# Performance work log

Measured on AMD Instinct MI355X. Metric: run time of the kernel, lower is better.

The kernel has to match this reference:

```python
import jax, jax.numpy as jnp
import numpy as np
from jax import lax

LATENT = 128
CODEBOOK = 1024

def _conv(x, w, b):
    # NCHW conv, kernel OIHW, stride 1, padding 1 (same)
    y = lax.conv_general_dilated(x, w, (1, 1), ((1, 1), (1, 1)),
                                 dimension_numbers=('NCHW', 'OIHW', 'NCHW'))
    return y + b[None, :, None, None]

def _conv_transpose(x, w, b):
    # ConvTranspose2d(k=3, s=1, p=1) == conv with flipped kernel, in/out swapped, pad 1
    w_eff = jnp.flip(w, (2, 3)).transpose(1, 0, 2, 3)  # [Cin,Cout,3,3] -> [Cout,Cin,3,3]
    return _conv(x, w_eff, b)

def _maxpool2(x):
    return lax.reduce_window(x, -jnp.inf, lax.max, (1, 1, 2, 2), (1, 1, 2, 2), 'VALID')

def _upsample2(x):
    # F.interpolate(scale_factor=2), default nearest
    return jnp.repeat(jnp.repeat(x, 2, axis=2), 2, axis=3)

def setup_inputs() -> dict:
    key = jax.random.key(0)
    ks = jax.random.split(key, 20)
    f = jnp.float32
    inp = {
        'x': jax.random.uniform(ks[0], (8192, 1, 24, 24), dtype=f),
        'conv1_w': jax.random.normal(ks[1], (32, 1, 3, 3), f) * 0.1,
        'conv1_b': jnp.zeros((32,), f),
        'conv2_w': jax.random.normal(ks[2], (64, 32, 3, 3), f) * 0.05,
        'conv2_b': jnp.zeros((64,), f),
        'conv3_w': jax.random.normal(ks[3], (128, 64, 3, 3), f) * 0.04,
        'conv3_b': jnp.zeros((128,), f),
        'enc_fc_w': jax.random.normal(ks[4], (LATENT, 3 * 3 * 128), f) * 0.03,
        'enc_fc_b': jnp.zeros((LATENT,), f),
        'codebook': jax.random.normal(ks[5], (CODEBOOK, LATENT), f),
        'dec_fc_w': jax.random.normal(ks[6], (3 * 3 * 128, LATENT), f) * 0.09,
        'dec_fc_b': jnp.zeros((3 * 3 * 128,), f),
        'dct1_w': jax.random.normal(ks[7], (128, 64, 3, 3), f) * 0.03,  # [Cin,Cout,kh,kw]
        'dct1_b': jnp.zeros((64,), f),
        'dct2_w': jax.random.normal(ks[8], (64, 32, 3, 3), f) * 0.04,
        'dct2_b': jnp.zeros((32,), f),
        'dct3_w': jax.random.normal(ks[9], (32, 1, 3, 3), f) * 0.06,
        'dct3_b': jnp.zeros((1,), f),
    }
    return inp

def reference(x, conv1_w, conv1_b, conv2_w, conv2_b, conv3_w, conv3_b,
              enc_fc_w, enc_fc_b, codebook, dec_fc_w, dec_fc_b,
              dct1_w, dct1_b, dct2_w, dct2_b, dct3_w, dct3_b):
    # ---- Encoder ----
    h = _maxpool2(jax.nn.relu(_conv(x, conv1_w, conv1_b)))     # [B,32,12,12]
    h = _maxpool2(jax.nn.relu(_conv(h, conv2_w, conv2_b)))     # [B,64,6,6]
    h = _maxpool2(jax.nn.relu(_conv(h, conv3_w, conv3_b)))     # [B,128,3,3]
    z = h.reshape(-1, 3 * 3 * 128) @ enc_fc_w.T + enc_fc_b     # [B,128]
    # ---- Quantize (L2 nearest-codeword; matmul-trick distances, same argmin) ----
    d2 = (jnp.sum(z * z, axis=1, keepdims=True)
          - 2.0 * z @ codebook.T
          + jnp.sum(codebook * codebook, axis=1)[None, :])     # [B,K]
    idx = jnp.argmin(d2, axis=1)                               # [B]
    z_q = codebook[idx]                                        # [B,128]
    # ---- Decoder ----
    d = z_q @ dec_fc_w.T + dec_fc_b                            # [B,1152]
    d = d.reshape(-1, 128, 3, 3)
    d = _upsample2(jax.nn.relu(_conv_transpose(d, dct1_w, dct1_b)))  # [B,64,6,6]
    d = _upsample2(jax.nn.relu(_conv_transpose(d, dct2_w, dct2_b)))  # [B,32,12,12]
    d = _upsample2(jax.nn.relu(_conv_transpose(d, dct3_w, dct3_b)))  # [B,1,24,24]
    return d
```

## Files before the change

kernel.cpp:

```cpp
#include <hip/hip_runtime.h>

typedef __attribute__((ext_vector_type(8))) short short8;
typedef __attribute__((ext_vector_type(4))) float f32x4;
typedef unsigned short ushort_t;
typedef unsigned int uint_t;

#define OFF_W1R   0
#define OFF_BD2F  288
#define OFF_BD1F  18720
#define OFF_EWT   (18720+73728)
#define OFF_CT    (92448+147456)
#define OFF_CC    (239904+131072)
#define OFF_DWT   (370976+1024)
#define OFF_D1R   (372000+147456)
#define OFF_D2R   (519456+73728)
#define OFF_D3R   (593184+18432)
#define WS_WEIGHTS (611616+288)
#define OFF_W2BF  WS_WEIGHTS
#define OFF_W3BF  (OFF_W2BF+18432)
#define OFF_H     (OFF_W3BF+73728)
#define OFF_TABLE OFF_H
#define OFF_IDSN  (OFF_H+8192*1152)

__device__ __forceinline__ ushort_t f2bf(float v) {
  uint_t u = __float_as_uint(v);
  return (ushort_t)((u + 0x7FFFu + ((u >> 16) & 1u)) >> 16);
}
__device__ __forceinline__ float bf2f(ushort_t b) {
  return __uint_as_float(((uint_t)b) << 16);
}

__global__ void vq_prep(const float* __restrict__ conv1_w, const float* __restrict__ codebook,
                        const float* __restrict__ dec_fc_w, const float* __restrict__ dct3_w,
                        float* __restrict__ ws) {
  int i = blockIdx.x * blockDim.x + threadIdx.x;
  if (i >= WS_WEIGHTS) return;
  if (i < OFF_BD2F) {
    int tap = i >> 5, co = i & 31;
    ws[i] = conv1_w[co*9 + tap];
  } else if (i < OFF_CC) {
    return;
  } else if (i < OFF_DWT) {
    int k = i - OFF_CC;
    float s = 0.f;
    for (int j = 0; j < 128; ++j) { float v = codebook[k*128+j]; s += v*v; }
    ws[i] = s;
  } else if (i < OFF_D1R) {
    int l = i - OFF_DWT;
    int j = l % 1152, k = l / 1152;
    ws[i] = dec_fc_w[j*128 + k];
  } else if (i < OFF_D3R) {
    return;
  } else if (i < WS_WEIGHTS) {
    int l = i - OFF_D3R;
    int tap = l % 9, ci = l / 9;
    ws[i] = dct3_w[ci*9 + (8 - tap)];
  }
}

#define P2_N (92160 + 294912 + 262144 + 73728 + 18432)
__global__ void vq_prep2(const float* __restrict__ conv2_w, const float* __restrict__ conv3_w,
                         const float* __restrict__ enc_fc_w, const float* __restrict__ codebook,
                         const float* __restrict__ dct1_w, const float* __restrict__ dct2_w,
                         float* __restrict__ ws) {
  int i = blockIdx.x * blockDim.x + threadIdx.x;
  if (i >= P2_N) return;
  ushort_t* W2  = (ushort_t*)(ws + OFF_W2BF);
  ushort_t* W3  = (ushort_t*)(ws + OFF_W3BF);
  ushort_t* EW  = (ushort_t*)(ws + OFF_EWT);
  ushort_t* CB  = (ushort_t*)(ws + OFF_CT);
  ushort_t* BD1 = (ushort_t*)(ws + OFF_BD1F);
  ushort_t* BD2 = (ushort_t*)(ws + OFF_BD2F);
  if (i < 18432) {
    int tap = i >> 11, r = i & 2047, co = r >> 5, ch = r & 31;
    float v = conv2_w[(co*32 + ch)*9 + tap];
    ushort_t hb = f2bf(v);
    W2[i] = hb; W2[18432 + i] = f2bf(v - bf2f(hb));
  } else if (i < 92160) {
    int j = i - 18432;
    int tap = j >> 13, r = j & 8191, co = r >> 6, ch = r & 63;
    float v = conv3_w[(co*64 + ch)*9 + tap];
    ushort_t hb = f2bf(v);
    W3[j] = hb; W3[73728 + j] = f2bf(v - bf2f(hb));
  } else if (i < 387072) {
    int r = i - 92160;
    int p = r / 147456; r %= 147456;
    int kk = r & 31, n = (r >> 5) & 127, ks = r >> 12;
    float v = enc_fc_w[n*1152 + ks*32 + kk];
    ushort_t hb = f2bf(v);
    if (p == 0) EW[r] = hb; else EW[147456 + r] = f2bf(v - bf2f(hb));
  } else if (i < 649216) {
    int r = i - 387072;
    int p = r / 131072; r %= 131072;
    int kk = r & 31, cw = (r >> 5) & 1023, ks = r >> 15;
    float v = codebook[cw*128 + ks*32 + kk];
    ushort_t hb = f2bf(v);
    if (p == 0) CB[r] = hb; else CB[131072 + r] = f2bf(v - bf2f(hb));
  } else if (i < 722944) {
    int r = i - 649216;
    int co = r / 1152, k = r - co*1152;
    int tap = k >> 7, ci = k & 127;
    float v = dct1_w[(ci*64 + co)*9 + (8 - tap)];
    ushort_t hb = f2bf(v);
    BD1[r] = hb; BD1[73728 + r] = f2bf(v - bf2f(hb));
  } else {
    int r = i - 722944;
    int co = r / 576, k = r - co*576;
    int tap = k >> 6, ci = k & 63;
    float v = dct2_w[(ci*32 + co)*9 + (8 - tap)];
    ushort_t hb = f2bf(v);
    BD2[r] = hb; BD2[18432 + r] = f2bf(v - bf2f(hb));
  }
}

__global__ __launch_bounds__(256, 3) void vq_enc(
    const float* __restrict__ x,
    const float* __restrict__ b1, const float* __restrict__ b2, const float* __restrict__ b3,
    const float* __restrict__ ws, ushort_t* __restrict__ hhi, ushort_t* __restrict__ hlo)
{
  __shared__ ushort_t R0h[6272], R0l[6272];
  __shared__ ushort_t A2h[5120], A2l[5120];
  __shared__ float XT[624];
  const int t = threadIdx.x;
  const int b = blockIdx.x;

  for (int i = t; i < 3136; i += 256) { ((uint_t*)R0h)[i] = 0u; ((uint_t*)R0l)[i] = 0u; }
  for (int i = t; i < 2560; i += 256) { ((uint_t*)A2h)[i] = 0u; ((uint_t*)A2l)[i] = 0u; }
  const float* xb = x + (size_t)b * 576;
  for (int i = t; i < 624; i += 256) {
    int row = i / 26, c = i - row * 26;
    XT[i] = (c >= 1 && c <= 24) ? xb[row*24 + c - 1] : 0.f;
  }
  __syncthreads();

  {
    int cp = t & 15, g = t >> 4;
    int gy = g >> 2, gx = g & 3;
    float wgt[2][9], bs[2];
    #pragma unroll
    for (int c = 0; c < 2; ++c) {
      bs[c] = b1[2*cp + c];
      #pragma unroll
      for (int k = 0; k < 9; ++k) wgt[c][k] = ws[OFF_W1R + k*32 + 2*cp + c];
    }
    int quadc = cp >> 2, coff = (cp & 3) * 2;
    #pragma unroll
    for (int pr = 0; pr < 3; ++pr) {
      int Y = (gy*3 + pr)*2;
      float a0[2][6], a1[2][6];
      #pragma unroll
      for (int c = 0; c < 2; ++c)
        #pragma unroll
        for (int i = 0; i < 6; ++i) { a0[c][i] = 0.f; a1[c][i] = 0.f; }
      #pragma unroll
      for (int wy = 0; wy < 4; ++wy) {
        int ry = Y - 1 + wy;
        if (ry < 0 || ry > 23) continue;
        const float2* rp = (const float2*)&XT[ry*26 + gx*6];
        float r[8];
        #pragma unroll
        for (int k = 0; k < 4; ++k) { float2 p = rp[k]; r[2*k] = p.x; r[2*k+1] = p.y; }
        if (wy < 3) {
          #pragma unroll
          for (int c = 0; c < 2; ++c)
            #pragma unroll
            for (int xx = 0; xx < 6; ++xx)
              #pragma unroll
              for (int dx = 0; dx < 3; ++dx) a0[c][xx] += r[xx+dx] * wgt[c][wy*3+dx];
        }
        if (wy >= 1) {
          #pragma unroll
          for (int c = 0; c < 2; ++c)
            #pragma unroll
            for (int xx = 0; xx < 6; ++xx)
              #pragma unroll
              for (int dx = 0; dx < 3; ++dx) a1[c][xx] += r[xx+dx] * wgt[c][(wy-1)*3+dx];
        }
      }
      #pragma unroll
      for (int pc = 0; pc < 3; ++pc) {
        uint_t hi = 0, lo = 0;
        #pragma unroll
        for (int c = 0; c < 2; ++c) {
          float m = fmaxf(fmaxf(a0[c][2*pc], a0[c][2*pc+1]), fmaxf(a1[c][2*pc], a1[c][2*pc+1]));
          float v = m + bs[c]; v = v > 0.f ? v : 0.f;
          ushort_t hb = f2bf(v);
          ushort_t lb = f2bf(v - bf2f(hb));
          hi |= ((uint_t)hb) << (16*c);
          lo |= ((uint_t)lb) << (16*c);
        }
        int p = (gy*3 + pr + 1)*14 + (gx*3 + pc + 1);
        int base = quadc*1568 + p*8 + coff;
        ((uint_t*)R0h)[base >> 1] = hi;
        ((uint_t*)R0l)[base >> 1] = lo;
      }
    }
  }
  __syncthreads();

  const int lane = t & 63, quad = lane >> 4, col = lane & 15;
  const int wv = t >> 6;

  {
    const int h = wv & 1, p = wv >> 1;
    const ushort_t* W2 = (const ushort_t*)(ws + OFF_W2BF);
    int pA[5];
    #pragma unroll
    for (int mi = 0; mi < 5; ++mi) {
      int m = (h*5 + mi)*16 + col; if (m > 143) m = 143;
      int cell = m >> 2, sub = m & 3;
      int opy = cell / 6, opx = cell - opy*6;
      int y = 2*opy + (sub >> 1), xx = 2*opx + (sub & 1);
      pA[mi] = y*14 + xx;
    }
    f32x4 acc[5][2];
    #pragma unroll
    for (int mi = 0; mi < 5; ++mi) { acc[mi][0] = (f32x4)0.f; acc[mi][1] = (f32x4)0.f; }
    const int co0 = p*32 + col, co1 = co0 + 16;
    #pragma unroll
    for (int t9 = 0; t9 < 9; ++t9) {
      const int toff = (t9/3)*14 + (t9%3);
      int bidx = t9*2048 + quad*8;
      short8 Bh0 = *(const short8*)(W2 + bidx + co0*32);
      short8 Bh1 = *(const short8*)(W2 + bidx + co1*32);
      short8 Bl0 = *(const short8*)(W2 + 18432 + bidx + co0*32);
      short8 Bl1 = *(const short8*)(W2 + 18432 + bidx + co1*32);
      #pragma unroll
      for (int mi = 0; mi < 5; ++mi) {
        int a = quad*1568 + (pA[mi] + toff)*8;
        short8 Ah = *(const short8*)(R0h + a);
        short8 Al = *(const short8*)(R0l + a);
        acc[mi][0] = __builtin_amdgcn_mfma_f32_16x16x32_bf16(Al, Bh0, acc[mi][0], 0, 0, 0);
        acc[mi][0] = __builtin_amdgcn_mfma_f32_16x16x32_bf16(Ah, Bl0, acc[mi][0], 0, 0, 0);
        acc[mi][0] = __builtin_amdgcn_mfma_f32_16x16x32_bf16(Ah, Bh0, acc[mi][0], 0, 0, 0);
        acc[mi][1] = __builtin_amdgcn_mfma_f32_16x16x32_bf16(Al, Bh1, acc[mi][1], 0, 0, 0);
        acc[mi][1] = __builtin_amdgcn_mfma_f32_16x16x32_bf16(Ah, Bl1, acc[mi][1], 0, 0, 0);
        acc[mi][1] = __builtin_amdgcn_mfma_f32_16x16x32_bf16(Ah, Bh1, acc[mi][1], 0, 0, 0);
      }
    }
    #pragma unroll
    for (int mi = 0; mi < 5; ++mi) {
      int cell = (h*5 + mi)*4 + quad;
      if (cell < 36) {
        int opy = cell / 6, opx = cell - opy*6;
        int p2 = (opy+1)*10 + (opx+1);
        #pragma unroll
        for (int j = 0; j < 2; ++j) {
          int ch = j ? co1 : co0;
          f32x4 a = acc[mi][j];
          float v = fmaxf(fmaxf(a.x, a.y), fmaxf(a.z, a.w)) + b2[ch];
          v = v > 0.f ? v : 0.f;
          ushort_t hb = f2bf(v);
          int wa = (ch >> 3)*640 + p2*8 + (ch & 7);
          A2h[wa] = hb;
          A2l[wa] = f2bf(v - bf2f(hb));
        }
      }
    }
  }
  __syncthreads();

  {
    const ushort_t* W3 = (const ushort_t*)(ws + OFF_W3BF);
    int pA[3];
    #pragma unroll
    for (int mt = 0; mt < 3; ++mt) {
      int m = mt*16 + col; if (m > 35) m = 35;
      int cell = m >> 2, sub = m & 3;
      int opy = cell / 3, opx = cell - opy*3;
      int y = 2*opy + (sub >> 1), xx = 2*opx + (sub & 1);
      pA[mt] = y*10 + xx;
    }
    f32x4 acc[3][2];
    #pragma unroll
    for (int mt = 0; mt < 3; ++mt) { acc[mt][0] = (f32x4)0.f; acc[mt][1] = (f32x4)0.f; }
    const int co0 = wv*16 + col, co1 = co0 + 64;
    #pragma unroll
    for (int ks = 0; ks < 18; ++ks) {
      const int t9 = ks >> 1, half = ks & 1, ch0 = half*32;
      const int toff = (t9/3)*10 + (t9%3);
      const int grp = half*4 + quad;
      int bidx = t9*8192 + ch0 + quad*8;
      short8 Bh0 = *(const short8*)(W3 + bidx + co0*64);
      short8 Bh1 = *(const short8*)(W3 + bidx + co1*64);
      short8 Bl0 = *(const short8*)(W3 + 73728 + bidx + co0*64);
      short8 Bl1 = *(const short8*)(W3 + 73728 + bidx + co1*64);
      #pragma unroll
      for (int mt = 0; mt < 3; ++mt) {
        int a = grp*640 + (pA[mt] + toff)*8;
        short8 Ah = *(const short8*)(A2h + a);
        short8 Al = *(const short8*)(A2l + a);
        acc[mt][0] = __builtin_amdgcn_mfma_f32_16x16x32_bf16(Al, Bh0, acc[mt][0], 0, 0, 0);
        acc[mt][0] = __builtin_amdgcn_mfma_f32_16x16x32_bf16(Ah, Bl0, acc[mt][0], 0, 0, 0);
        acc[mt][0] = __builtin_amdgcn_mfma_f32_16x16x32_bf16(Ah, Bh0, acc[mt][0], 0, 0, 0);
        acc[mt][1] = __builtin_amdgcn_mfma_f32_16x16x32_bf16(Al, Bh1, acc[mt][1], 0, 0, 0);
        acc[mt][1] = __builtin_amdgcn_mfma_f32_16x16x32_bf16(Ah, Bl1, acc[mt][1], 0, 0, 0);
        acc[mt][1] = __builtin_amdgcn_mfma_f32_16x16x32_bf16(Ah, Bh1, acc[mt][1], 0, 0, 0);
      }
    }
    ushort_t* hb_ = hhi + (size_t)b * 1152;
    ushort_t* lb_ = hlo + (size_t)b * 1152;
    #pragma unroll
    for (int mt = 0; mt < 3; ++mt) {
      int cell = mt*4 + quad;
      if (cell < 9) {
        #pragma unroll
        for (int j = 0; j < 2; ++j) {
          int ch = j ? co1 : co0;
          f32x4 a = acc[mt][j];
          float v = fmaxf(fmaxf(a.x, a.y), fmaxf(a.z, a.w)) + b3[ch];
          v = v > 0.f ? v : 0.f;
          ushort_t hb2 = f2bf(v);
          hb_[ch*9 + cell] = hb2;
          lb_[ch*9 + cell] = f2bf(v - bf2f(hb2));
        }
      }
    }
  }
}

__global__ __launch_bounds__(256, 4) void vq_fc_argmin(
    const float* __restrict__ efb, const float* __restrict__ ws,
    const ushort_t* __restrict__ hhi, const ushort_t* __restrict__ hlo,
    int* __restrict__ ids)
{
  __shared__ float ZL[16*132];
  __shared__ float WVs[64];
  __shared__ int   WIs[64];
  const int t = threadIdx.x;
  const int sb = blockIdx.x * 16;
  const int lane = t & 63, wv = t >> 6;
  const int col = lane & 15, quad = lane >> 4;

  const ushort_t* EW  = (const ushort_t*)(ws + OFF_EWT);
  const ushort_t* CBB = (const ushort_t*)(ws + OFF_CT);

  f32x4 acc0 = (f32x4)0.f, acc1 = (f32x4)0.f;
  const size_t hrow = (size_t)(sb + col) * 1152 + quad*8;
  #pragma unroll 4
  for (int ks = 0; ks < 36; ++ks) {
    short8 Ah = *(const short8*)(hhi + hrow + ks*32);
    short8 Al = *(const short8*)(hlo + hrow + ks*32);
    int n0 = wv*32 + col, n1 = n0 + 16;
    const ushort_t* bp0 = EW + (ks*128 + n0)*32 + quad*8;
    const ushort_t* bp1 = EW + (ks*128 + n1)*32 + quad*8;
    short8 Bh0 = *(const short8*)(bp0);
    short8 Bl0 = *(const short8*)(bp0 + 147456);
    short8 Bh1 = *(const short8*)(bp1);
    short8 Bl1 = *(const short8*)(bp1 + 147456);
    acc0 = __builtin_amdgcn_mfma_f32_16x16x32_bf16(Al, Bh0, acc0, 0, 0, 0);
    acc0 = __builtin_amdgcn_mfma_f32_16x16x32_bf16(Ah, Bl0, acc0, 0, 0, 0);
    acc0 = __builtin_amdgcn_mfma_f32_16x16x32_bf16(Ah, Bh0, acc0, 0, 0, 0);
    acc1 = __builtin_amdgcn_mfma_f32_16x16x32_bf16(Al, Bh1, acc1, 0, 0, 0);
    acc1 = __builtin_amdgcn_mfma_f32_16x16x32_bf16(Ah, Bl1, acc1, 0, 0, 0);
    acc1 = __builtin_amdgcn_mfma_f32_16x16x32_bf16(Ah, Bh1, acc1, 0, 0, 0);
  }
  {
    int n0 = wv*32 + col, n1 = n0 + 16;
    float bs0 = efb[n0], bs1 = efb[n1];
    #pragma unroll
    for (int r = 0; r < 4; ++r) {
      int m = quad*4 + r;
      ZL[m*132 + n0] = acc0[r] + bs0;
      ZL[m*132 + n1] = acc1[r] + bs1;
    }
  }
  __syncthreads();

  short8 zAh[4], zAl[4];
  #pragma unroll
  for (int ks = 0; ks < 4; ++ks) {
    const float* zp = &ZL[col*132 + ks*32 + quad*8];
    float4 z0 = *(const float4*)zp;
    float4 z1 = *(const float4*)(zp + 4);
    float zv[8] = {z0.x, z0.y, z0.z, z0.w, z1.x, z1.y, z1.z, z1.w};
    ushort_t ph[8], pl[8];
    #pragma unroll
    for (int e = 0; e < 8; ++e) {
      ushort_t hb = f2bf(zv[e]);
      ph[e] = hb; pl[e] = f2bf(zv[e] - bf2f(hb));
    }
    zAh[ks] = *(const short8*)ph;
    zAl[ks] = *(const short8*)pl;
  }

  float bestv[4]; int besti[4];
  #pragma unroll
  for (int r = 0; r < 4; ++r) { bestv[r] = 3.4e38f; besti[r] = 0; }
  for (int c4 = 0; c4 < 4; ++c4) {
    f32x4 dacc[4];
    #pragma unroll
    for (int nn = 0; nn < 4; ++nn) dacc[nn] = (f32x4)0.f;
    #pragma unroll
    for (int ks = 0; ks < 4; ++ks) {
      #pragma unroll
      for (int nn = 0; nn < 4; ++nn) {
        int cw = (wv*16 + c4*4 + nn)*16 + col;
        const ushort_t* bp = CBB + (size_t)(ks*1024 + cw)*32 + quad*8;
        short8 Bh = *(const short8*)bp;
        short8 Bl = *(const short8*)(bp + 131072);
        dacc[nn] = __builtin_amdgcn_mfma_f32_16x16x32_bf16(zAl[ks], Bh, dacc[nn], 0, 0, 0);
        dacc[nn] = __builtin_amdgcn_mfma_f32_16x16x32_bf16(zAh[ks], Bl, dacc[nn], 0, 0, 0);
        dacc[nn] = __builtin_amdgcn_mfma_f32_16x16x32_bf16(zAh[ks], Bh, dacc[nn], 0, 0, 0);
      }
    }
    #pragma unroll
    for (int nn = 0; nn < 4; ++nn) {
      int cw = (wv*16 + c4*4 + nn)*16 + col;
      float ccv = ws[OFF_CC + cw];
      #pragma unroll
      for (int r = 0; r < 4; ++r) {
        float dist = ccv - 2.f*dacc[nn][r];
        if (dist < bestv[r]) { bestv[r] = dist; besti[r] = cw; }
      }
    }
  }

  #pragma unroll
  for (int r = 0; r < 4; ++r) {
    float v = bestv[r]; int ii = besti[r];
    #pragma unroll
    for (int off = 8; off >= 1; off >>= 1) {
      float v2 = __shfl_xor(v, off); int i2 = __shfl_xor(ii, off);
      if (v2 < v || (v2 == v && i2 < ii)) { v = v2; ii = i2; }
    }
    if (col == 0) {
      int m = quad*4 + r;
      WVs[wv*16 + m] = v; WIs[wv*16 + m] = ii;
    }
  }
  __syncthreads();
  if (t < 16) {
    float v = WVs[t]; int ii = WIs[t];
    #pragma unroll
    for (int w2 = 1; w2 < 4; ++w2) {
      float v2 = WVs[w2*16 + t]; int i2 = WIs[w2*16 + t];
      if (v2 < v || (v2 == v && i2 < ii)) { v = v2; ii = i2; }
    }
    ids[sb + t] = ii;
  }
}

__global__ __launch_bounds__(256, 4) void vq_dec_table(
    const float* __restrict__ codebook, const float* __restrict__ decb,
    const float* __restrict__ d1b, const float* __restrict__ d2b, const float* __restrict__ d3b,
    const float* __restrict__ ws, float* __restrict__ table)
{
  __shared__ float POOL[8008];
  __shared__ float PS[1536];
  __shared__ float ZQ[128];
  ushort_t* FAh = (ushort_t*)POOL;
  ushort_t* FAl = FAh + 3400;
  ushort_t* GAh = (ushort_t*)(POOL + 3400);
  ushort_t* GAl = GAh + 4608;
  float* R2 = POOL;

  const int t = threadIdx.x;
  const int cw = blockIdx.x;
  const int lane = t & 63, wv = t >> 6;
  const int col = lane & 15, quad = lane >> 4;

  for (int i = t; i < 8008; i += 256) POOL[i] = 0.f;
  if (t < 128) ZQ[t] = codebook[(size_t)cw*128 + t];
  __syncthreads();

  #pragma unroll
  for (int p = 0; p < 5; ++p) {
    int j = t + p*256;
    if (j < 1152) {
      float a0 = decb[j];
      const float* wb = ws + OFF_DWT + j;
      #pragma unroll 4
      for (int k = 0; k < 128; ++k) a0 += wb[k*1152] * ZQ[k];
      int ci = j / 9, rem = j - ci*9;
      int pix = ((rem/3)+1)*5 + (rem%3) + 1;
      ushort_t hb = f2bf(a0);
      FAh[pix*136 + ci] = hb;
      FAl[pix*136 + ci] = f2bf(a0 - bf2f(hb));
    }
  }
  __syncthreads();

  const ushort_t* BD1 = (const ushort_t*)(ws + OFF_BD1F);
  f32x4 acc1 = (f32x4)0.f;
  {
    const int m9 = col < 9 ? col : 8;
    const int oy = m9/3, ox = m9 - oy*3;
    const int co = wv*16 + col;
    #pragma unroll 4
    for (int ks = 0; ks < 36; ++ks) {
      int kb = ks*32 + quad*8;
      int tap = kb >> 7, ci0 = kb & 127;
      int pix = (oy + tap/3)*5 + ox + tap%3;
      short8 Ah = *(const short8*)(FAh + pix*136 + ci0);
      short8 Al = *(const short8*)(FAl + pix*136 + ci0);
      const ushort_t* bp = BD1 + co*1152 + kb;
      short8 Bh = *(const short8*)bp;
      short8 Bl = *(const short8*)(bp + 73728);
      acc1 = __builtin_amdgcn_mfma_f32_16x16x32_bf16(Al, Bh, acc1, 0, 0, 0);
      acc1 = __builtin_amdgcn_mfma_f32_16x16x32_bf16(Ah, Bl, acc1, 0, 0, 0);
      acc1 = __builtin_amdgcn_mfma_f32_16x16x32_bf16(Ah, Bh, acc1, 0, 0, 0);
    }
  }
  {
    const int co = wv*16 + col;
    float bias = d1b[co];
    #pragma unroll
    for (int r = 0; r < 4; ++r) {
      int m = quad*4 + r;
      if (m < 9) {
        int oy = m/3, ox = m - oy*3;
        float v = acc1[r] + bias; v = v > 0.f ? v : 0.f;
        ushort_t hb = f2bf(v), lb = f2bf(v - bf2f(hb));
        int rbase = (2*oy+1)*8 + (2*ox+1);
        GAh[(rbase  )*72 + co] = hb; GAh[(rbase+1)*72 + co] = hb;
        GAh[(rbase+8)*72 + co] = hb; GAh[(rbase+9)*72 + co] = hb;
        GAl[(rbase  )*72 + co] = lb; GAl[(rbase+1)*72 + co] = lb;
        GAl[(rbase+8)*72 + co] = lb; GAl[(rbase+9)*72 + co] = lb;
      }
    }
  }
  __syncthreads();

  const ushort_t* BD2 = (const ushort_t*)(ws + OFF_BD2F);
  f32x4 acc2[3];
  acc2[0] = (f32x4)0.f; acc2[1] = (f32x4)0.f; acc2[2] = (f32x4)0.f;
  const int h = wv >> 1, js = (wv & 1)*3;
  for (int ks = h*9; ks < h*9 + 9; ++ks) {
    int kb = ks*32 + quad*8;
    int tap = kb >> 6, ci0 = kb & 63;
    int ty = tap/3, tx = tap - ty*3;
    #pragma unroll
    for (int jj = 0; jj < 3; ++jj) {
      int job = js + jj;
      int mt = job >> 1, nt = job & 1;
      int m = mt*16 + col; if (m > 35) m = 35;
      int oy = m/6, ox = m - oy*6;
      int pix = (oy+ty)*8 + ox+tx;
      short8 Ah = *(const short8*)(GAh + pix*72 + ci0);
      short8 Al = *(const short8*)(GAl + pix*72 + ci0);
      int co = nt*16 + col;
      const ushort_t* bp = BD2 + co*576 + kb;
      short8 Bh = *(const short8*)bp;
      short8 Bl = *(const short8*)(bp + 18432);
      acc2[jj] = __builtin_amdgcn_mfma_f32_16x16x32_bf16(Al, Bh, acc2[jj], 0, 0, 0);
      acc2[jj] = __builtin_amdgcn_mfma_f32_16x16x32_bf16(Ah, Bl, acc2[jj], 0, 0, 0);
      acc2[jj] = __builtin_amdgcn_mfma_f32_16x16x32_bf16(Ah, Bh, acc2[jj], 0, 0, 0);
    }
  }
  __syncthreads();
  if (h == 1) {
    #pragma unroll
    for (int jj = 0; jj < 3; ++jj) {
      int job = js + jj;
      #pragma unroll
      for (int r = 0; r < 4; ++r) PS[(job*64 + lane)*4 + r] = acc2[jj][r];
    }
  }
  for (int i = t; i < 6468; i += 256) R2[i] = 0.f;
  __syncthreads();
  if (h == 0) {
    #pragma unroll
    for (int jj = 0; jj < 3; ++jj) {
      int job = js + jj;
      int mt = job >> 1, nt = job & 1;
      int co = nt*16 + col;
      float bias = d2b[co];
      #pragma unroll
      for (int r = 0; r < 4; ++r) {
        float v = acc2[jj][r] + PS[(job*64 + lane)*4 + r];
        int m = mt*16 + quad*4 + r;
        if (m < 36) {
          int oy = m/6, ox = m - oy*6;
          v += bias; v = v > 0.f ? v : 0.f;
          int rbase = (2*oy+1)*14 + (2*ox+1);
          R2[(rbase   )*33 + co] = v; R2[(rbase+ 1)*33 + co] = v;
          R2[(rbase+14)*33 + co] = v; R2[(rbase+15)*33 + co] = v;
        }
      }
    }
  }
  __syncthreads();

  if (t < 144) {
    int yy = t / 12, xx = t - yy*12;
    const float* w3 = ws + OFF_D3R;
    float acc = d3b[0];
    #pragma unroll
    for (int dy = 0; dy < 3; ++dy)
      #pragma unroll
      for (int dx = 0; dx < 3; ++dx) {
        const float* rp = &R2[((yy+dy)*14 + xx+dx)*33];
        const float* wp = w3 + dy*3 + dx;
        #pragma unroll 8
        for (int ci = 0; ci < 32; ++ci) acc += rp[ci] * wp[ci*9];
      }
    float v = acc > 0.f ? acc : 0.f;
    float* ob = table + (size_t)cw * 576;
    int o0 = (2*yy)*24 + 2*xx;
    ob[o0] = v; ob[o0+1] = v; ob[o0+24] = v; ob[o0+25] = v;
  }
}

__global__ __launch_bounds__(256, 8) void vq_scatter(
    const float* __restrict__ table, const int* __restrict__ ids,
    float* __restrict__ out, int nvec)
{
  int idx = blockIdx.x * 256 + threadIdx.x;
  if (idx >= nvec) return;
  int b = idx / 144;
  int r = idx - b * 144;
  int cw = ids[b];
  ((float4*)out)[idx] = ((const float4*)(table + (size_t)cw * 576))[r];
}

extern "C" void kernel_launch(void* const* d_in, const int* in_sizes, int n_in,
                              void* d_out, int out_size, void* d_ws, size_t ws_size,
                              hipStream_t stream) {
  const float* x   = (const float*)d_in[0];
  const float* c1w = (const float*)d_in[1];
  const float* c1b = (const float*)d_in[2];
  const float* c2w = (const float*)d_in[3];
  const float* c2b = (const float*)d_in[4];
  const float* c3w = (const float*)d_in[5];
  const float* c3b = (const float*)d_in[6];
  const float* efw = (const float*)d_in[7];
  const float* efb = (const float*)d_in[8];
  const float* cb  = (const float*)d_in[9];
  const float* dfw = (const float*)d_in[10];
  const float* dfb = (const float*)d_in[11];
  const float* dw1 = (const float*)d_in[12];
  const float* db1 = (const float*)d_in[13];
  const float* dw2 = (const float*)d_in[14];
  const float* db2 = (const float*)d_in[15];
  const float* dw3 = (const float*)d_in[16];
  const float* db3 = (const float*)d_in[17];
  float* ws = (float*)d_ws;
  ushort_t* hhi  = (ushort_t*)(ws + OFF_H);
  ushort_t* hlo  = hhi + (size_t)8192*1152;
  float* table = ws + OFF_TABLE;
  int*   ids   = (int*)(ws + OFF_IDSN);
  float* outp = (float*)d_out;
  int B = in_sizes[0] / 576;

  vq_prep<<<(WS_WEIGHTS + 255) / 256, 256, 0, stream>>>(c1w, cb, dfw, dw3, ws);
  vq_prep2<<<(P2_N + 255) / 256, 256, 0, stream>>>(c2w, c3w, efw, cb, dw1, dw2, ws);
  vq_enc<<<B, 256, 0, stream>>>(x, c1b, c2b, c3b, ws, hhi, hlo);
  vq_fc_argmin<<<B/16, 256, 0, stream>>>(efb, ws, hhi, hlo, ids);
  vq_dec_table<<<1024, 256, 0, stream>>>(cb, dfb, db1, db2, db3, ws, table);
  int nvec = B * 144;
  vq_scatter<<<(nvec + 255) / 256, 256, 0, stream>>>(table, ids, outp, nvec);
}
```

Measured before the change: 633.2 us.

## Restructure encoder LDS layouts with padded channel stride and alias conv3 buffer

Merges the two weight-prep kernels into a single launch. The encoder's conv1 output moves from a channel-group-major layout to a pixel-major layout with padded channel stride (40), and the conv2 output reuses the same LDS buffer with a stride of 72. Conv1 is remapped so each thread handles one channel over 12 columns. Dropping the separate A2 buffers lowers LDS use, which is meant to allow 4 blocks per CU instead of 3. The cost is an extra barrier and a re-zeroing pass, and the new strides may change LDS bank-conflict behaviour.

```diff
diff --git a/kernel.cpp b/kernel.cpp
--- a/kernel.cpp
+++ b/kernel.cpp
@@ -13,7 +13,6 @@
 #define OFF_CC    (239904+131072)
 #define OFF_DWT   (370976+1024)
 #define OFF_D1R   (372000+147456)
-#define OFF_D2R   (519456+73728)
 #define OFF_D3R   (593184+18432)
 #define WS_WEIGHTS (611616+288)
 #define OFF_W2BF  WS_WEIGHTS
@@ -30,41 +29,41 @@
   return __uint_as_float(((uint_t)b) << 16);
 }
 
-__global__ void vq_prep(const float* __restrict__ conv1_w, const float* __restrict__ codebook,
-                        const float* __restrict__ dec_fc_w, const float* __restrict__ dct3_w,
-                        float* __restrict__ ws) {
-  int i = blockIdx.x * blockDim.x + threadIdx.x;
-  if (i >= WS_WEIGHTS) return;
-  if (i < OFF_BD2F) {
-    int tap = i >> 5, co = i & 31;
-    ws[i] = conv1_w[co*9 + tap];
-  } else if (i < OFF_CC) {
+#define P2_N (92160 + 294912 + 262144 + 73728 + 18432)
+#define PREP_N (WS_WEIGHTS + P2_N)
+__global__ void vq_prep_all(const float* __restrict__ conv1_w, const float* __restrict__ conv2_w,
+                            const float* __restrict__ conv3_w, const float* __restrict__ enc_fc_w,
+                            const float* __restrict__ codebook, const float* __restrict__ dec_fc_w,
+                            const float* __restrict__ dct1_w, const float* __restrict__ dct2_w,
+                            const float* __restrict__ dct3_w, float* __restrict__ ws) {
+  int i0 = blockIdx.x * blockDim.x + threadIdx.x;
+  if (i0 >= PREP_N) return;
+  if (i0 < WS_WEIGHTS) {
+    int i = i0;
+    if (i < OFF_BD2F) {
+      int tap = i >> 5, co = i & 31;
+      ws[i] = conv1_w[co*9 + tap];
+    } else if (i < OFF_CC) {
+      return;
+    } else if (i < OFF_DWT) {
+      int k = i - OFF_CC;
+      float s = 0.f;
+      for (int j = 0; j < 128; ++j) { float v = codebook[k*128+j]; s += v*v; }
+      ws[i] = s;
+    } else if (i < OFF_D1R) {
+      int l = i - OFF_DWT;
+      int j = l % 1152, k = l / 1152;
+      ws[i] = dec_fc_w[j*128 + k];
+    } else if (i < OFF_D3R) {
+      return;
+    } else {
+      int l = i - OFF_D3R;
+      int tap = l % 9, ci = l / 9;
+      ws[i] = dct3_w[ci*9 + (8 - tap)];
+    }
     return;
-  } else if (i < OFF_DWT) {
-    int k = i - OFF_CC;
-    float s = 0.f;
-    for (int j = 0; j < 128; ++j) { float v = codebook[k*128+j]; s += v*v; }
-    ws[i] = s;
-  } else if (i < OFF_D1R) {
-    int l = i - OFF_DWT;
-    int j = l % 1152, k = l / 1152;
-    ws[i] = dec_fc_w[j*128 + k];
-  } else if (i < OFF_D3R) {
-    return;
-  } else if (i < WS_WEIGHTS) {
-    int l = i - OFF_D3R;
-    int tap = l % 9, ci = l / 9;
-    ws[i] = dct3_w[ci*9 + (8 - tap)];
-  }
-}
-
-#define P2_N (92160 + 294912 + 262144 + 73728 + 18432)
-__global__ void vq_prep2(const float* __restrict__ conv2_w, const float* __restrict__ conv3_w,
-                         const float* __restrict__ enc_fc_w, const float* __restrict__ codebook,
-                         const float* __restrict__ dct1_w, const float* __restrict__ dct2_w,
-                         float* __restrict__ ws) {
-  int i = blockIdx.x * blockDim.x + threadIdx.x;
-  if (i >= P2_N) return;
+  }
+  int i = i0 - WS_WEIGHTS;
   ushort_t* W2  = (ushort_t*)(ws + OFF_W2BF);
   ushort_t* W3  = (ushort_t*)(ws + OFF_W3BF);
   ushort_t* EW  = (ushort_t*)(ws + OFF_EWT);
@@ -113,86 +112,68 @@
   }
 }
 
-__global__ __launch_bounds__(256, 3) void vq_enc(
+__global__ __launch_bounds__(256, 4) void vq_enc(
     const float* __restrict__ x,
     const float* __restrict__ b1, const float* __restrict__ b2, const float* __restrict__ b3,
     const float* __restrict__ ws, ushort_t* __restrict__ hhi, ushort_t* __restrict__ hlo)
 {
-  __shared__ ushort_t R0h[6272], R0l[6272];
-  __shared__ ushort_t A2h[5120], A2l[5120];
+  __shared__ ushort_t R0h[7840], R0l[7840];
   __shared__ float XT[624];
+  ushort_t* C3h = R0h;
+  ushort_t* C3l = R0l;
   const int t = threadIdx.x;
   const int b = blockIdx.x;
 
-  for (int i = t; i < 3136; i += 256) { ((uint_t*)R0h)[i] = 0u; ((uint_t*)R0l)[i] = 0u; }
-  for (int i = t; i < 2560; i += 256) { ((uint_t*)A2h)[i] = 0u; ((uint_t*)A2l)[i] = 0u; }
+  for (int i = t; i < 3920; i += 256) { ((uint_t*)R0h)[i] = 0u; ((uint_t*)R0l)[i] = 0u; }
   const float* xb = x + (size_t)b * 576;
   for (int i = t; i < 624; i += 256) {
-    int row = i / 26, c = i - row * 26;
-    XT[i] = (c >= 1 && c <= 24) ? xb[row*24 + c - 1] : 0.f;
+    int row = i / 26, col = i - row * 26;
+    XT[i] = (col >= 1 && col <= 24) ? xb[row*24 + col - 1] : 0.f;
   }
   __syncthreads();
 
   {
-    int cp = t & 15, g = t >> 4;
-    int gy = g >> 2, gx = g & 3;
-    float wgt[2][9], bs[2];
-    #pragma unroll
-    for (int c = 0; c < 2; ++c) {
-      bs[c] = b1[2*cp + c];
-      #pragma unroll
-      for (int k = 0; k < 9; ++k) wgt[c][k] = ws[OFF_W1R + k*32 + 2*cp + c];
-    }
-    int quadc = cp >> 2, coff = (cp & 3) * 2;
+    int co = t & 31, g = t >> 5, gy = g >> 1, gx = g & 1;
+    float w[9];
+    #pragma unroll
+    for (int k = 0; k < 9; ++k) w[k] = ws[OFF_W1R + k*32 + co];
+    float bias = b1[co];
     #pragma unroll
     for (int pr = 0; pr < 3; ++pr) {
-      int Y = (gy*3 + pr)*2;
-      float a0[2][6], a1[2][6];
-      #pragma unroll
-      for (int c = 0; c < 2; ++c)
-        #pragma unroll
-        for (int i = 0; i < 6; ++i) { a0[c][i] = 0.f; a1[c][i] = 0.f; }
+      int Y = gy*6 + pr*2;
+      float a0[12], a1[12];
+      #pragma unroll
+      for (int i = 0; i < 12; ++i) { a0[i] = 0.f; a1[i] = 0.f; }
       #pragma unroll
       for (int wy = 0; wy < 4; ++wy) {
         int ry = Y - 1 + wy;
         if (ry < 0 || ry > 23) continue;
-        const float2* rp = (const float2*)&XT[ry*26 + gx*6];
-        float r[8];
+        const float2* rp = (const float2*)&XT[ry*26 + gx*12];
+        float r[14];
         #pragma unroll
-        for (int k = 0; k < 4; ++k) { float2 p = rp[k]; r[2*k] = p.x; r[2*k+1] = p.y; }
+        for (int k = 0; k < 7; ++k) { float2 p = rp[k]; r[2*k] = p.x; r[2*k+1] = p.y; }
         if (wy < 3) {
           #pragma unroll
-          for (int c = 0; c < 2; ++c)
+          for (int xx = 0; xx < 12; ++xx)
             #pragma unroll
-            for (int xx = 0; xx < 6; ++xx)
-              #pragma unroll
-              for (int dx = 0; dx < 3; ++dx) a0[c][xx] += r[xx+dx] * wgt[c][wy*3+dx];
+            for (int dx = 0; dx < 3; ++dx) a0[xx] += r[xx+dx] * w[wy*3+dx];
         }
         if (wy >= 1) {
           #pragma unroll
-          for (int c = 0; c < 2; ++c)
+          for (int xx = 0; xx < 12; ++xx)
             #pragma unroll
-            for (int xx = 0; xx < 6; ++xx)
-              #pragma unroll
-              for (int dx = 0; dx < 3; ++dx) a1[c][xx] += r[xx+dx] * wgt[c][(wy-1)*3+dx];
+            for (int dx = 0; dx < 3; ++dx) a1[xx] += r[xx+dx] * w[(wy-1)*3+dx];
         }
       }
       #pragma unroll
-      for (int pc = 0; pc < 3; ++pc) {
-        uint_t hi = 0, lo = 0;
-        #pragma unroll
-        for (int c = 0; c < 2; ++c) {
-          float m = fmaxf(fmaxf(a0[c][2*pc], a0[c][2*pc+1]), fmaxf(a1[c][2*pc], a1[c][2*pc+1]));
-          float v = m + bs[c]; v = v > 0.f ? v : 0.f;
-          ushort_t hb = f2bf(v);
-          ushort_t lb = f2bf(v - bf2f(hb));
-          hi |= ((uint_t)hb) << (16*c);
-          lo |= ((uint_t)lb) << (16*c);
-        }
-        int p = (gy*3 + pr + 1)*14 + (gx*3 + pc + 1);
-        int base = quadc*1568 + p*8 + coff;
-        ((uint_t*)R0h)[base >> 1] = hi;
-        ((uint_t*)R0l)[base >> 1] = lo;
+      for (int pc = 0; pc < 6; ++pc) {
+        float m = fmaxf(fmaxf(a0[2*pc], a0[2*pc+1]), fmaxf(a1[2*pc], a1[2*pc+1]));
+        float v = m + bias; v = v > 0.f ? v : 0.f;
+        int row = gy*3 + pr, colp = gx*6 + pc;
+        int addr = ((row+1)*14 + (colp+1))*40 + co;
+        ushort_t hb = f2bf(v);
+        R0h[addr] = hb;
+        R0l[addr] = f2bf(v - bf2f(hb));
       }
     }
   }
@@ -204,14 +185,14 @@
   {
     const int h = wv & 1, p = wv >> 1;
     const ushort_t* W2 = (const ushort_t*)(ws + OFF_W2BF);
-    int pA[5];
+    int baseA[5];
     #pragma unroll
     for (int mi = 0; mi < 5; ++mi) {
       int m = (h*5 + mi)*16 + col; if (m > 143) m = 143;
       int cell = m >> 2, sub = m & 3;
       int opy = cell / 6, opx = cell - opy*6;
       int y = 2*opy + (sub >> 1), xx = 2*opx + (sub & 1);
-      pA[mi] = y*14 + xx;
+      baseA[mi] = (y*14 + xx)*40 + quad*8;
     }
     f32x4 acc[5][2];
     #pragma unroll
@@ -219,7 +200,7 @@
     const int co0 = p*32 + col, co1 = co0 + 16;
     #pragma unroll
     for (int t9 = 0; t9 < 9; ++t9) {
-      const int toff = (t9/3)*14 + (t9%3);
+      const int TAPOFF = ((t9/3)*14 + (t9%3))*40;
       int bidx = t9*2048 + quad*8;
       short8 Bh0 = *(const short8*)(W2 + bidx + co0*32);
       short8 Bh1 = *(const short8*)(W2 + bidx + co1*32);
@@ -227,7 +208,7 @@
       short8 Bl1 = *(const short8*)(W2 + 18432 + bidx + co1*32);
       #pragma unroll
       for (int mi = 0; mi < 5; ++mi) {
-        int a = quad*1568 + (pA[mi] + toff)*8;
+        int a = baseA[mi] + TAPOFF;
         short8 Ah = *(const short8*)(R0h + a);
         short8 Al = *(const short8*)(R0l + a);
         acc[mi][0] = __builtin_amdgcn_mfma_f32_16x16x32_bf16(Al, Bh0, acc[mi][0], 0, 0, 0);
@@ -238,12 +219,15 @@
         acc[mi][1] = __builtin_amdgcn_mfma_f32_16x16x32_bf16(Ah, Bh1, acc[mi][1], 0, 0, 0);
       }
     }
+    __syncthreads();
+    for (int i = t; i < 2304; i += 256) { ((uint_t*)C3h)[i] = 0u; ((uint_t*)C3l)[i] = 0u; }
+    __syncthreads();
     #pragma unroll
     for (int mi = 0; mi < 5; ++mi) {
       int cell = (h*5 + mi)*4 + quad;
       if (cell < 36) {
         int opy = cell / 6, opx = cell - opy*6;
-        int p2 = (opy+1)*10 + (opx+1);
+        int wa = ((opy+1)*8 + (opx+1))*72;
         #pragma unroll
         for (int j = 0; j < 2; ++j) {
           int ch = j ? co1 : co0;
@@ -251,9 +235,8 @@
           float v = fmaxf(fmaxf(a.x, a.y), fmaxf(a.z, a.w)) + b2[ch];
           v = v > 0.f ? v : 0.f;
           ushort_t hb = f2bf(v);
-          int wa = (ch >> 3)*640 + p2*8 + (ch & 7);
-          A2h[wa] = hb;
-          A2l[wa] = f2bf(v - bf2f(hb));
+          C3h[wa + ch] = hb;
+          C3l[wa + ch] = f2bf(v - bf2f(hb));
         }
       }
     }
@@ -262,14 +245,14 @@
 
   {
     const ushort_t* W3 = (const ushort_t*)(ws + OFF_W3BF);
-    int pA[3];
+    int baseA[3];
     #pragma unroll
     for (int mt = 0; mt < 3; ++mt) {
       int m = mt*16 + col; if (m > 35) m = 35;
       int cell = m >> 2, sub = m & 3;
       int opy = cell / 3, opx = cell - opy*3;
       int y = 2*opy + (sub >> 1), xx = 2*opx + (sub & 1);
-      pA[mt] = y*10 + xx;
+      baseA[mt] = (y*8 + xx)*72 + quad*8;
     }
     f32x4 acc[3][2];
     #pragma unroll
@@ -277,9 +260,8 @@
     const int co0 = wv*16 + col, co1 = co0 + 64;
     #pragma unroll
     for (int ks = 0; ks < 18; ++ks) {
-      const int t9 = ks >> 1, half = ks & 1, ch0 = half*32;
-      const int toff = (t9/3)*10 + (t9%3);
-      const int grp = half*4 + quad;
+      const int t9 = ks >> 1, ch0 = (ks & 1)*32;
+      const int TAPOFF = ((t9/3)*8 + (t9%3))*72;
       int bidx = t9*8192 + ch0 + quad*8;
       short8 Bh0 = *(const short8*)(W3 + bidx + co0*64);
       short8 Bh1 = *(const short8*)(W3 + bidx + co1*64);
@@ -287,9 +269,9 @@
       short8 Bl1 = *(const short8*)(W3 + 73728 + bidx + co1*64);
       #pragma unroll
       for (int mt = 0; mt < 3; ++mt) {
-        int a = grp*640 + (pA[mt] + toff)*8;
-        short8 Ah = *(const short8*)(A2h + a);
-        short8 Al = *(const short8*)(A2l + a);
+        int a = baseA[mt] + TAPOFF + ch0;
+        short8 Ah = *(const short8*)(C3h + a);
+        short8 Al = *(const short8*)(C3l + a);
         acc[mt][0] = __builtin_amdgcn_mfma_f32_16x16x32_bf16(Al, Bh0, acc[mt][0], 0, 0, 0);
         acc[mt][0] = __builtin_amdgcn_mfma_f32_16x16x32_bf16(Ah, Bl0, acc[mt][0], 0, 0, 0);
         acc[mt][0] = __builtin_amdgcn_mfma_f32_16x16x32_bf16(Ah, Bh0, acc[mt][0], 0, 0, 0);
@@ -643,8 +625,7 @@
   float* outp = (float*)d_out;
   int B = in_sizes[0] / 576;
 
-  vq_prep<<<(WS_WEIGHTS + 255) / 256, 256, 0, stream>>>(c1w, cb, dfw, dw3, ws);
-  vq_prep2<<<(P2_N + 255) / 256, 256, 0, stream>>>(c2w, c3w, efw, cb, dw1, dw2, ws);
+  vq_prep_all<<<(PREP_N + 255) / 256, 256, 0, stream>>>(c1w, c2w, c3w, efw, cb, dfw, dw1, dw2, dw3, ws);
   vq_enc<<<B, 256, 0, stream>>>(x, c1b, c2b, c3b, ws, hhi, hlo);
   vq_fc_argmin<<<B/16, 256, 0, stream>>>(efb, ws, hhi, hlo, ids);
   vq_dec_table<<<1024, 256, 0, stream>>>(cb, dfb, db1, db2, db3, ws, table);
```

Result: no change. 627.4 us (-0.9%).
